# Performance work log

Hardware: AMD Instinct MI355X
Metric: run time of the kernel (lower is better)

Reference implementation:

```python
import jax, jax.numpy as jnp
import numpy as np

VOCAB = 32000
D = 1024
B, S = 4, 2048


def setup_inputs() -> dict:
    key = jax.random.key(0)
    k_ids, k_w = jax.random.split(key)
    token_ids = jax.random.randint(k_ids, (B, S), 0, VOCAB, dtype=jnp.int64 if jax.config.jax_enable_x64 else jnp.int32)
    # trunc_normal_(0, 1, -3, 3) ~ truncated standard normal in [-3, 3]
    weight = jax.random.truncated_normal(k_w, -3.0, 3.0, (VOCAB, D), dtype=jnp.float32)
    return {"token_ids": token_ids, "weight": weight}


def reference(token_ids, weight) -> jnp.ndarray:
    # Original: one_hot(token_ids, V) @ weight  ==  weight[token_ids] (a gather).
    # [B, S] int -> [B, S, D]
    return jnp.take(weight, token_ids, axis=0)
```

## Files before the change

### kernel.cpp

```cpp
#include <hip/hip_runtime.h>
#include <hip/hip_bf16.h>


#define D_DIM 1024

__global__ __launch_bounds__(256) void embed_gather_kernel(
    const int* __restrict__ ids,
    const float* __restrict__ weight,
    float* __restrict__ out,
    int n_tokens)
{
    const int t = blockIdx.x;
    if (t >= n_tokens) return;

    const int row = ids[t];

    const float4* __restrict__ src =
        reinterpret_cast<const float4*>(weight + (size_t)row * D_DIM);
    float4* __restrict__ dst =
        reinterpret_cast<float4*>(out + (size_t)t * D_DIM);

    dst[threadIdx.x] = src[threadIdx.x];
}

extern "C" void kernel_launch(void* const* d_in, const int* in_sizes, int n_in,
                              void* d_out, int out_size, void* d_ws, size_t ws_size,
                              hipStream_t stream) {
    const int*   ids    = (const int*)d_in[0];
    const float* weight = (const float*)d_in[1];
    float*       out    = (float*)d_out;

    const int n_tokens = in_sizes[0];

    embed_gather_kernel<<<n_tokens, 256, 0, stream>>>(ids, weight, out, n_tokens);
}
```

Baseline: 179.8 us.

## Map one wave per token row, two rows per wave with batched loads

Each 64-lane wave now copies a whole 4 KB embedding row instead of one block handling a row, and each wave handles two tokens. All eight float4 loads are issued before any store so more memory requests are in flight per thread. The grid shrinks eightfold, which cuts block launch overhead but may lower the number of resident waves available to hide latency.

```diff
diff --git a/kernel.cpp b/kernel.cpp
--- a/kernel.cpp
+++ b/kernel.cpp
@@ -1,5 +1,4 @@
 #include <hip/hip_runtime.h>
-#include <hip/hip_bf16.h>
 
 
 #define D_DIM 1024
@@ -10,17 +9,34 @@
     float* __restrict__ out,
     int n_tokens)
 {
-    const int t = blockIdx.x;
-    if (t >= n_tokens) return;
+    const int lane = (int)(threadIdx.x & 63u);
+    const int wave = (int)(threadIdx.x >> 6);
+    const int nwaves = (int)gridDim.x * 4;
+    const int t0 = (int)blockIdx.x * 4 + wave;
+    const int t1 = t0 + nwaves;
 
-    const int row = ids[t];
+    if (t0 >= n_tokens) return;
+    const bool has1 = (t1 < n_tokens);
 
-    const float4* __restrict__ src =
-        reinterpret_cast<const float4*>(weight + (size_t)row * D_DIM);
-    float4* __restrict__ dst =
-        reinterpret_cast<float4*>(out + (size_t)t * D_DIM);
+    const int row0 = ids[t0];
+    const int row1 = has1 ? ids[t1] : row0;
 
-    dst[threadIdx.x] = src[threadIdx.x];
+    const float4* __restrict__ s0 =
+        reinterpret_cast<const float4*>(weight + (size_t)row0 * D_DIM) + lane;
+    const float4* __restrict__ s1 =
+        reinterpret_cast<const float4*>(weight + (size_t)row1 * D_DIM) + lane;
+    float4* __restrict__ d0 =
+        reinterpret_cast<float4*>(out + (size_t)t0 * D_DIM) + lane;
+    float4* __restrict__ d1 =
+        reinterpret_cast<float4*>(out + (size_t)t1 * D_DIM) + lane;
+
+    float4 a0 = s0[0], a1 = s0[64], a2 = s0[128], a3 = s0[192];
+    float4 b0 = s1[0], b1 = s1[64], b2 = s1[128], b3 = s1[192];
+
+    d0[0]   = a0; d0[64]  = a1; d0[128] = a2; d0[192] = a3;
+    if (has1) {
+        d1[0]   = b0; d1[64]  = b1; d1[128] = b2; d1[192] = b3;
+    }
 }
 
 extern "C" void kernel_launch(void* const* d_in, const int* in_sizes, int n_in,
@@ -32,5 +48,6 @@
 
     const int n_tokens = in_sizes[0];
 
-    embed_gather_kernel<<<n_tokens, 256, 0, stream>>>(ids, weight, out, n_tokens);
+    const int blocks = (n_tokens + 7) / 8;
+    embed_gather_kernel<<<blocks, 256, 0, stream>>>(ids, weight, out, n_tokens);
 }
```

Result: no change. 178.6 us (-0.7%).
